# Kernel tuning notes

Measured on AMD Instinct MI355X. Metric: run time of the kernel, lower is better.

The kernel has to match this reference:

```python
import jax, jax.numpy as jnp
import numpy as np

IN_DIM, OUT_DIM = 4096, 11008
NUM_SUBDIM, KS = 1376, 256
DS = OUT_DIM // NUM_SUBDIM  # 8
BATCH = 32


def setup_inputs() -> dict:
    key = jax.random.key(0)
    k1, k2, k3, k4 = jax.random.split(key, 4)
    x = jax.random.normal(k1, (BATCH, IN_DIM), dtype=jnp.float32)
    vectors = jax.random.normal(k2, (NUM_SUBDIM, KS, DS), dtype=jnp.float32)
    bias = jax.random.normal(k3, (OUT_DIM,), dtype=jnp.float32)
    indexes = jax.random.randint(k4, (IN_DIM, NUM_SUBDIM), 0, KS, dtype=jnp.int64)
    return {"x": x, "vectors": vectors, "bias": bias, "indexes": indexes}


def reference(x, vectors, bias, indexes):
    in_dim, num_subdim = indexes.shape
    ds = vectors.shape[-1]
    # PQ dequant: gather codewords per (row, subspace) -> [in_dim, num_subdim, Ds]
    # vectors[d, indexes[i, d]] via broadcast of arange(num_subdim) against indexes.
    dims = jnp.arange(num_subdim)
    weight = vectors[dims, indexes].reshape(in_dim, num_subdim * ds)  # [in_dim, out_dim]
    return x @ weight + bias
```

## Files before the change

kernel.cpp:

```cpp
#include <hip/hip_runtime.h>

#define IN_DIM  4096
#define OUT_DIM 11008
#define NSUB    1376
#define KSQ     256
#define DSUB    8
#define BATCH   32

#define DTILE   16
#define NTILE   128
#define KC      128
#define KSPLIT  16
#define KPB     (IN_DIM / KSPLIT)
#define NCHUNK  (KPB / KC)
#define NBLK    (OUT_DIM / NTILE)

typedef unsigned short ushort_t;
typedef unsigned int   uint_t;
typedef __attribute__((ext_vector_type(8))) short bf16x8;
typedef __attribute__((ext_vector_type(4))) float f32x4;

#define SW_STRIDE 136
#define SX_STRIDE 136
#define SI_STRIDE 132

#define VEC_N   (NSUB * KSQ * DSUB)
#define XBF_OFF 5636096
#define PREP_V  (VEC_N / 2)
#define PREP_X  (BATCH * IN_DIM / 2)
#define PREP_O  (BATCH * OUT_DIM)
#define PREP_N  (PREP_V + PREP_X + PREP_O)

__device__ __forceinline__ ushort_t f2bf(float f) {
    union { float f; uint_t u; } a; a.f = f;
    uint_t u = a.u;
    u += 0x7fffu + ((u >> 16) & 1u);
    return (ushort_t)(u >> 16);
}

__global__ __launch_bounds__(256) void pq_prep(
    const float* __restrict__ x, const float* __restrict__ vecs,
    const float* __restrict__ bias,
    uint_t* __restrict__ vbf, uint_t* __restrict__ xbf, float* __restrict__ out)
{
    int tid = blockIdx.x * 256 + threadIdx.x;
    if (tid < PREP_V) {
        float2 v = ((const float2*)vecs)[tid];
        vbf[tid] = (uint_t)f2bf(v.x) | ((uint_t)f2bf(v.y) << 16);
    } else if (tid < PREP_V + PREP_X) {
        int i = tid - PREP_V;
        float2 v = ((const float2*)x)[i];
        xbf[i] = (uint_t)f2bf(v.x) | ((uint_t)f2bf(v.y) << 16);
    } else {
        int i = tid - (PREP_V + PREP_X);
        out[i] = bias[i % OUT_DIM];
    }
}

__global__ __launch_bounds__(256) void pq_main(
    const ushort_t* __restrict__ xbf, const uint4* __restrict__ vbf,
    const int* __restrict__ idx, float* __restrict__ out)
{
    __shared__ ushort_t sW[NTILE * SW_STRIDE];
    __shared__ ushort_t sX[BATCH * SX_STRIDE];
    __shared__ int      sI[DTILE * SI_STRIDE];

    const int t    = threadIdx.x;
    const int nblk = blockIdx.x;
    const int kblk = blockIdx.y;
    const int d0   = nblk * DTILE;
    const int kbase = kblk * KPB;

    const int wave = t >> 6;
    const int lane = t & 63;
    const int l15  = lane & 15;
    const int l4   = lane >> 4;

    const int gd = t >> 4;
    const int go = t & 15;

    f32x4 acc[2][2];
    #pragma unroll
    for (int i = 0; i < 2; ++i)
        #pragma unroll
        for (int j = 0; j < 2; ++j)
            acc[i][j] = (f32x4)0.0f;

    int   ireg[8];
    uint4 xreg[2];

    {
        const int i0 = kbase;
        #pragma unroll
        for (int p = 0; p < 8; ++p) {
            int f = p * 256 + t, ii = f >> 4, dd = f & 15;
            ireg[p] = idx[(size_t)(i0 + ii) * NSUB + (d0 + dd)];
        }
        #pragma unroll
        for (int p = 0; p < 2; ++p) {
            int f = p * 256 + t, b = f >> 4, q = f & 15;
            xreg[p] = ((const uint4*)xbf)[b * (IN_DIM / 8) + i0 / 8 + q];
        }
    }

    for (int c = 0; c < NCHUNK; ++c) {
        __syncthreads();

        #pragma unroll
        for (int p = 0; p < 8; ++p) {
            int f = p * 256 + t, ii = f >> 4, dd = f & 15;
            sI[dd * SI_STRIDE + ii] = ireg[p];
        }
        #pragma unroll
        for (int p = 0; p < 2; ++p) {
            int f = p * 256 + t, b = f >> 4, q = f & 15;
            *(uint4*)&sX[b * SX_STRIDE + q * 8] = xreg[p];
        }
        __syncthreads();

        int kk[8];
        #pragma unroll
        for (int s = 0; s < 8; ++s)
            kk[s] = sI[gd * SI_STRIDE + go * 8 + s];

        uint4 q[8];
        #pragma unroll
        for (int s = 0; s < 8; ++s)
            q[s] = vbf[(d0 + gd) * KSQ + kk[s]];

        if (c + 1 < NCHUNK) {
            const int i0n = kbase + (c + 1) * KC;
            #pragma unroll
            for (int p = 0; p < 8; ++p) {
                int f = p * 256 + t, ii = f >> 4, dd = f & 15;
                ireg[p] = idx[(size_t)(i0n + ii) * NSUB + (d0 + dd)];
            }
            #pragma unroll
            for (int p = 0; p < 2; ++p) {
                int f = p * 256 + t, b = f >> 4, qq = f & 15;
                xreg[p] = ((const uint4*)xbf)[b * (IN_DIM / 8) + i0n / 8 + qq];
            }
        }

        #pragma unroll
        for (int j = 0; j < 8; ++j) {
            const uint_t sel = (j & 1) ? 0x07060302u : 0x05040100u;
            uint_t c0 = (j >> 1) == 0 ? q[0].x : (j >> 1) == 1 ? q[0].y : (j >> 1) == 2 ? q[0].z : q[0].w;
            uint_t c1 = (j >> 1) == 0 ? q[1].x : (j >> 1) == 1 ? q[1].y : (j >> 1) == 2 ? q[1].z : q[1].w;
            uint_t c2 = (j >> 1) == 0 ? q[2].x : (j >> 1) == 1 ? q[2].y : (j >> 1) == 2 ? q[2].z : q[2].w;
            uint_t c3 = (j >> 1) == 0 ? q[3].x : (j >> 1) == 1 ? q[3].y : (j >> 1) == 2 ? q[3].z : q[3].w;
            uint_t c4 = (j >> 1) == 0 ? q[4].x : (j >> 1) == 1 ? q[4].y : (j >> 1) == 2 ? q[4].z : q[4].w;
            uint_t c5 = (j >> 1) == 0 ? q[5].x : (j >> 1) == 1 ? q[5].y : (j >> 1) == 2 ? q[5].z : q[5].w;
            uint_t c6 = (j >> 1) == 0 ? q[6].x : (j >> 1) == 1 ? q[6].y : (j >> 1) == 2 ? q[6].z : q[6].w;
            uint_t c7 = (j >> 1) == 0 ? q[7].x : (j >> 1) == 1 ? q[7].y : (j >> 1) == 2 ? q[7].z : q[7].w;
            uint4 wv;
            wv.x = __builtin_amdgcn_perm(c1, c0, sel);
            wv.y = __builtin_amdgcn_perm(c3, c2, sel);
            wv.z = __builtin_amdgcn_perm(c5, c4, sel);
            wv.w = __builtin_amdgcn_perm(c7, c6, sel);
            *(uint4*)&sW[(gd * 8 + j) * SW_STRIDE + go * 8] = wv;
        }
        __syncthreads();

        #pragma unroll
        for (int kq = 0; kq < KC / 32; ++kq) {
            bf16x8 A[2], B[2];
            #pragma unroll
            for (int mt = 0; mt < 2; ++mt)
                A[mt] = *(const bf16x8*)
                    &sX[(mt * 16 + l15) * SX_STRIDE + kq * 32 + l4 * 8];
            #pragma unroll
            for (int nt = 0; nt < 2; ++nt)
                B[nt] = *(const bf16x8*)
                    &sW[(wave * 32 + nt * 16 + l15) * SW_STRIDE + kq * 32 + l4 * 8];
            #pragma unroll
            for (int mt = 0; mt < 2; ++mt)
                #pragma unroll
                for (int nt = 0; nt < 2; ++nt)
                    acc[mt][nt] = __builtin_amdgcn_mfma_f32_16x16x32_bf16(
                        A[mt], B[nt], acc[mt][nt], 0, 0, 0);
        }
    }

    #pragma unroll
    for (int mt = 0; mt < 2; ++mt)
        #pragma unroll
        for (int nt = 0; nt < 2; ++nt)
            #pragma unroll
            for (int r = 0; r < 4; ++r) {
                int row = mt * 16 + l4 * 4 + r;
                int col = nblk * NTILE + wave * 32 + nt * 16 + l15;
                atomicAdd(&out[(size_t)row * OUT_DIM + col], acc[mt][nt][r]);
            }
}

extern "C" void kernel_launch(void* const* d_in, const int* in_sizes, int n_in,
                              void* d_out, int out_size, void* d_ws, size_t ws_size,
                              hipStream_t stream) {
    const float* x    = (const float*)d_in[0];
    const float* vecs = (const float*)d_in[1];
    const float* bias = (const float*)d_in[2];
    const int*   idx  = (const int*)d_in[3];
    float* out = (float*)d_out;

    uint_t* vbf = (uint_t*)d_ws;
    uint_t* xbf = (uint_t*)((char*)d_ws + XBF_OFF);

    pq_prep<<<PREP_N / 256, 256, 0, stream>>>(x, vecs, bias, vbf, xbf, out);
    dim3 grid(NBLK, KSPLIT);
    pq_main<<<grid, 256, 0, stream>>>((const ushort_t*)xbf, (const uint4*)vbf,
                                      idx, out);
}
```

Measured before the change: 113.6 us.

## Double-buffer index and activation tiles and overlap MFMA with codeword gather

Index and activation tiles in LDS are now double-buffered, and the MFMA on the previous chunk's weight tile runs while the current chunk's codeword gather loads are in flight. This drops one barrier per chunk. The K-split is halved, so each block does more chunks and fewer atomic adds go to the output. The cost is more LDS use and fewer blocks in the grid, which may hurt latency hiding on a large GPU.

```diff
diff --git a/kernel.cpp b/kernel.cpp
--- a/kernel.cpp
+++ b/kernel.cpp
@@ -10,7 +10,7 @@
 #define DTILE   16
 #define NTILE   128
 #define KC      128
-#define KSPLIT  16
+#define KSPLIT  8
 #define KPB     (IN_DIM / KSPLIT)
 #define NCHUNK  (KPB / KC)
 #define NBLK    (OUT_DIM / NTILE)
@@ -57,13 +57,69 @@
     }
 }
 
+
+__device__ __forceinline__ void load_chunk(
+    const int* __restrict__ idx, const ushort_t* __restrict__ xbf,
+    int i0, int d0, int t, int (&ireg)[8], uint4 (&xreg)[2])
+{
+    #pragma unroll
+    for (int p = 0; p < 8; ++p) {
+        int f = p * 256 + t, ii = f >> 4, dd = f & 15;
+        ireg[p] = idx[(size_t)(i0 + ii) * NSUB + (d0 + dd)];
+    }
+    #pragma unroll
+    for (int p = 0; p < 2; ++p) {
+        int f = p * 256 + t, b = f >> 4, q = f & 15;
+        xreg[p] = ((const uint4*)xbf)[b * (IN_DIM / 8) + i0 / 8 + q];
+    }
+}
+
+__device__ __forceinline__ void commit_chunk(
+    int* sIbuf, ushort_t* sXbuf, int t,
+    const int (&ireg)[8], const uint4 (&xreg)[2])
+{
+    #pragma unroll
+    for (int p = 0; p < 8; ++p) {
+        int f = p * 256 + t, ii = f >> 4, dd = f & 15;
+        sIbuf[dd * SI_STRIDE + ii] = ireg[p];
+    }
+    #pragma unroll
+    for (int p = 0; p < 2; ++p) {
+        int f = p * 256 + t, b = f >> 4, q = f & 15;
+        *(uint4*)&sXbuf[b * SX_STRIDE + q * 8] = xreg[p];
+    }
+}
+
+__device__ __forceinline__ void mfma_chunk(
+    const ushort_t* __restrict__ sx, const ushort_t* __restrict__ sw,
+    f32x4 (&acc)[2][2], int l15, int l4, int wave)
+{
+    #pragma unroll
+    for (int kq = 0; kq < KC / 32; ++kq) {
+        bf16x8 A[2], B[2];
+        #pragma unroll
+        for (int mt = 0; mt < 2; ++mt)
+            A[mt] = *(const bf16x8*)&sx[(mt * 16 + l15) * SX_STRIDE + kq * 32 + l4 * 8];
+        #pragma unroll
+        for (int nt = 0; nt < 2; ++nt)
+            B[nt] = *(const bf16x8*)&sw[(wave * 32 + nt * 16 + l15) * SW_STRIDE + kq * 32 + l4 * 8];
+        #pragma unroll
+        for (int mt = 0; mt < 2; ++mt)
+            #pragma unroll
+            for (int nt = 0; nt < 2; ++nt)
+                acc[mt][nt] = __builtin_amdgcn_mfma_f32_16x16x32_bf16(
+                    A[mt], B[nt], acc[mt][nt], 0, 0, 0);
+    }
+}
+
+
 __global__ __launch_bounds__(256) void pq_main(
     const ushort_t* __restrict__ xbf, const uint4* __restrict__ vbf,
     const int* __restrict__ idx, float* __restrict__ out)
 {
     __shared__ ushort_t sW[NTILE * SW_STRIDE];
-    __shared__ ushort_t sX[BATCH * SX_STRIDE];
-    __shared__ int      sI[DTILE * SI_STRIDE];
+    __shared__ ushort_t sX[2][BATCH * SX_STRIDE];
+    __shared__ int      sI[2][DTILE * SI_STRIDE];
 
     const int t    = threadIdx.x;
     const int nblk = blockIdx.x;
@@ -89,58 +145,31 @@
     int   ireg[8];
     uint4 xreg[2];
 
-    {
-        const int i0 = kbase;
-        #pragma unroll
-        for (int p = 0; p < 8; ++p) {
-            int f = p * 256 + t, ii = f >> 4, dd = f & 15;
-            ireg[p] = idx[(size_t)(i0 + ii) * NSUB + (d0 + dd)];
-        }
-        #pragma unroll
-        for (int p = 0; p < 2; ++p) {
-            int f = p * 256 + t, b = f >> 4, q = f & 15;
-            xreg[p] = ((const uint4*)xbf)[b * (IN_DIM / 8) + i0 / 8 + q];
-        }
-    }
-
+    load_chunk(idx, xbf, kbase, d0, t, ireg, xreg);
+    commit_chunk(&sI[0][0], &sX[0][0], t, ireg, xreg);
+    load_chunk(idx, xbf, kbase + KC, d0, t, ireg, xreg);
+
+    #pragma unroll
     for (int c = 0; c < NCHUNK; ++c) {
         __syncthreads();
 
-        #pragma unroll
-        for (int p = 0; p < 8; ++p) {
-            int f = p * 256 + t, ii = f >> 4, dd = f & 15;
-            sI[dd * SI_STRIDE + ii] = ireg[p];
-        }
-        #pragma unroll
-        for (int p = 0; p < 2; ++p) {
-            int f = p * 256 + t, b = f >> 4, q = f & 15;
-            *(uint4*)&sX[b * SX_STRIDE + q * 8] = xreg[p];
-        }
+        const int* sic = &sI[c & 1][0];
+        int4 ka = *(const int4*)&sic[gd * SI_STRIDE + go * 8];
+        int4 kb = *(const int4*)&sic[gd * SI_STRIDE + go * 8 + 4];
+        uint4 q[8];
+        q[0] = vbf[(d0 + gd) * KSQ + ka.x];
+        q[1] = vbf[(d0 + gd) * KSQ + ka.y];
+        q[2] = vbf[(d0 + gd) * KSQ + ka.z];
+        q[3] = vbf[(d0 + gd) * KSQ + ka.w];
+        q[4] = vbf[(d0 + gd) * KSQ + kb.x];
+        q[5] = vbf[(d0 + gd) * KSQ + kb.y];
+        q[6] = vbf[(d0 + gd) * KSQ + kb.z];
+        q[7] = vbf[(d0 + gd) * KSQ + kb.w];
+
+        if (c > 0)
+            mfma_chunk(&sX[(c - 1) & 1][0], sW, acc, l15, l4, wave);
+
         __syncthreads();
-
-        int kk[8];
-        #pragma unroll
-        for (int s = 0; s < 8; ++s)
-            kk[s] = sI[gd * SI_STRIDE + go * 8 + s];
-
-        uint4 q[8];
-        #pragma unroll
-        for (int s = 0; s < 8; ++s)
-            q[s] = vbf[(d0 + gd) * KSQ + kk[s]];
-
-        if (c + 1 < NCHUNK) {
-            const int i0n = kbase + (c + 1) * KC;
-            #pragma unroll
-            for (int p = 0; p < 8; ++p) {
-                int f = p * 256 + t, ii = f >> 4, dd = f & 15;
-                ireg[p] = idx[(size_t)(i0n + ii) * NSUB + (d0 + dd)];
-            }
-            #pragma unroll
-            for (int p = 0; p < 2; ++p) {
-                int f = p * 256 + t, b = f >> 4, qq = f & 15;
-                xreg[p] = ((const uint4*)xbf)[b * (IN_DIM / 8) + i0n / 8 + qq];
-            }
-        }
 
         #pragma unroll
         for (int j = 0; j < 8; ++j) {
@@ -160,27 +189,14 @@
             wv.w = __builtin_amdgcn_perm(c7, c6, sel);
             *(uint4*)&sW[(gd * 8 + j) * SW_STRIDE + go * 8] = wv;
         }
-        __syncthreads();
-
-        #pragma unroll
-        for (int kq = 0; kq < KC / 32; ++kq) {
-            bf16x8 A[2], B[2];
-            #pragma unroll
-            for (int mt = 0; mt < 2; ++mt)
-                A[mt] = *(const bf16x8*)
-                    &sX[(mt * 16 + l15) * SX_STRIDE + kq * 32 + l4 * 8];
-            #pragma unroll
-            for (int nt = 0; nt < 2; ++nt)
-                B[nt] = *(const bf16x8*)
-                    &sW[(wave * 32 + nt * 16 + l15) * SW_STRIDE + kq * 32 + l4 * 8];
-            #pragma unroll
-            for (int mt = 0; mt < 2; ++mt)
-                #pragma unroll
-                for (int nt = 0; nt < 2; ++nt)
-                    acc[mt][nt] = __builtin_amdgcn_mfma_f32_16x16x32_bf16(
-                        A[mt], B[nt], acc[mt][nt], 0, 0, 0);
-        }
-    }
+
+        if (c + 1 < NCHUNK)
+            commit_chunk(&sI[(c + 1) & 1][0], &sX[(c + 1) & 1][0], t, ireg, xreg);
+        if (c + 2 < NCHUNK)
+            load_chunk(idx, xbf, kbase + (c + 2) * KC, d0, t, ireg, xreg);
+    }
+
+    mfma_chunk(&sX[(NCHUNK - 1) & 1][0], sW, acc, l15, l4, wave);
 
     #pragma unroll
     for (int mt = 0; mt < 2; ++mt)
```

Result: slower. 124.8 us (+9.8%).
